# Performance work log

Measured on AMD Instinct MI355X. Metric: run time of the kernel, lower is better.

The kernel has to match this reference:

```python
import jax, jax.numpy as jnp
import numpy as np

WINDOW = 512
OVERLAP = 64
STRIDE = WINDOW - OVERLAP  # 448
HEADS = 12
HEAD_DIM = 3072 // HEADS  # 256
SCALE = 1.0 / np.sqrt(HEAD_DIM)


def setup_inputs() -> dict:
    key = jax.random.key(0)
    ks = jax.random.split(key, 9)
    B, S, H = 1, 8192, 3072
    w = 0.02  # weight init scale
    return {
        "hidden_states": jax.random.normal(ks[0], (B, S, H), jnp.float32),
        "Wq": jax.random.normal(ks[1], (H, H), jnp.float32) * w,
        "bq": jnp.zeros((H,), jnp.float32),
        "Wk": jax.random.normal(ks[2], (H, H), jnp.float32) * w,
        "bk": jnp.zeros((H,), jnp.float32),
        "Wv": jax.random.normal(ks[3], (H, H), jnp.float32) * w,
        "bv": jnp.zeros((H,), jnp.float32),
        "Wo": jax.random.normal(ks[4], (H, H), jnp.float32) * w,
        "bo": jnp.zeros((H,), jnp.float32),
    }


def reference(hidden_states, Wq, bq, Wk, bk, Wv, bv, Wo, bo):
    B, S, H = hidden_states.shape
    n_win = -(-S // STRIDE)  # ceil: windows start at 0, STRIDE, 2*STRIDE, ... < S
    starts = np.arange(n_win) * STRIDE                      # static
    idx = starts[:, None] + np.arange(WINDOW)[None, :]      # [n_win, W]
    valid = jnp.asarray(idx < S)                            # [n_win, W] bool
    idx_c = np.minimum(idx, S - 1)                          # clamp for gather

    # Gather overlapping windows: [B, n_win, W, H] (redundant QKV on overlap, as in original)
    win = hidden_states[:, idx_c]

    def proj(Wm, bm):
        y = jnp.einsum('bnwh,oh->bnwo', win, Wm) + bm
        return y.reshape(B, n_win, WINDOW, HEADS, HEAD_DIM)

    q = proj(Wq, bq)
    k = proj(Wk, bk)
    v = proj(Wv, bv)

    scores = jnp.einsum('bnqhd,bnkhd->bnhqk', q, k) * SCALE  # [B,n_win,heads,W,W]
    # Padded (out-of-range) key positions of the short last window must not attend
    scores = jnp.where(valid[None, :, None, None, :], scores, -1e9)
    attn = jax.nn.softmax(scores, axis=-1)
    ctx = jnp.einsum('bnhqk,bnkhd->bnqhd', attn, v)
    ctx = ctx.reshape(B, n_win, WINDOW, H)
    out_w = jnp.einsum('bnwh,oh->bnwo', ctx, Wo) + bo        # [B,n_win,W,H]

    # zero padded query rows, then overlap-add + average
    out_w = out_w * valid[None, :, :, None].astype(out_w.dtype)
    flat_idx = jnp.asarray(idx_c.reshape(-1))                # [n_win*W]
    output = jnp.zeros((B, S, H), out_w.dtype).at[:, flat_idx].add(
        out_w.reshape(B, -1, H))
    counts = jnp.zeros((S,), out_w.dtype).at[flat_idx].add(
        valid.reshape(-1).astype(out_w.dtype))
    return output / jnp.maximum(counts, 1.0)[None, :, None]
```

## Files before the change

### kernel.cpp

```cpp
#include <hip/hip_runtime.h>
#include <hip/hip_bf16.h>
#include <stdint.h>

#define SEQ   8192
#define HDIM  3072
#define NWIN  19
#define WINL  512
#define STR   448
#define NHEAD 12
#define DHEAD 256
#define QKVN  9216
#define ATTN_SCALE 0.0625f

typedef unsigned short u16;
typedef __bf16 bf16x8 __attribute__((ext_vector_type(8)));
typedef float  f32x4  __attribute__((ext_vector_type(4)));
typedef unsigned short us8 __attribute__((ext_vector_type(8)));

__device__ __forceinline__ u16 f2b(float x) {
  return __builtin_bit_cast(u16, __float2bfloat16(x));
}
__device__ __forceinline__ float b2f(u16 u) {
  return __builtin_bit_cast(float, (unsigned int)(u) << 16);
}
__device__ __forceinline__ void gload_lds16(const void* g, void* l) {
  __builtin_amdgcn_global_load_lds(
      (const __attribute__((address_space(1))) void*)g,
      (__attribute__((address_space(3))) void*)l, 16, 0, 0);
}

__global__ __launch_bounds__(256) void cvt_f32_bf16(const float* __restrict__ src,
                                                    u16* __restrict__ dst, int n8) {
  int i = blockIdx.x * 256 + threadIdx.x;
  if (i >= n8) return;
  const float4* s4 = (const float4*)src;
  float4 a = s4[2 * i], b = s4[2 * i + 1];
  us8 o;
  o[0] = f2b(a.x); o[1] = f2b(a.y); o[2] = f2b(a.z); o[3] = f2b(a.w);
  o[4] = f2b(b.x); o[5] = f2b(b.y); o[6] = f2b(b.z); o[7] = f2b(b.w);
  *((us8*)dst + i) = o;
}

__global__ __launch_bounds__(256) void biascat(const float* __restrict__ bq,
                                               const float* __restrict__ bk,
                                               const float* __restrict__ bv,
                                               float* __restrict__ dst) {
  int i = blockIdx.x * 256 + threadIdx.x;
  if (i >= QKVN) return;
  dst[i] = (i < HDIM) ? bq[i] : ((i < 2 * HDIM) ? bk[i - HDIM] : bv[i - 2 * HDIM]);
}

template <bool BF16OUT>
__global__ __launch_bounds__(512, 2) void gemm256(const u16* __restrict__ A,
                                                  const u16* __restrict__ B,
                                                  const float* __restrict__ bias,
                                                  float* __restrict__ outF,
                                                  u16* __restrict__ outB,
                                                  int N, int K) {
  __shared__ __align__(16) u16 As[4][8192];
  __shared__ __align__(16) u16 Bs[4][8192];
  const int tid = threadIdx.x;
  const int w = tid >> 6, l = tid & 63;
  const int wm = w >> 2, wn = w & 3;
  const int fr = l & 15, g = l >> 4;
  const int xcd = blockIdx.x & 7, loc = blockIdx.x >> 3;
  const int bn = loc >> 2, bm = xcd * 4 + (loc & 3);

  const u16* Ab = A + (size_t)bm * 256 * K;
  const u16* Bb = B + (size_t)bn * 256 * K;

  const int r_st = w * 16 + (l >> 2);
  const int s_st = ((l & 3) ^ ((l >> 3) & 3)) * 8;
  const int sw = (g ^ ((fr >> 1) & 3)) * 8;

  f32x4 acc[8][4];
#pragma unroll
  for (int i = 0; i < 8; ++i)
#pragma unroll
    for (int j = 0; j < 4; ++j) acc[i][j] = (f32x4){0.f, 0.f, 0.f, 0.f};

  auto stA = [&](int T) {
    const int s = T & 3;
#pragma unroll
    for (int h = 0; h < 2; ++h)
      gload_lds16(Ab + (size_t)(h * 128 + r_st) * K + T * 32 + s_st,
                  (char*)&As[s][0] + h * 8192 + w * 1024 + l * 16);
  };
  auto stB = [&](int T) {
    const int s = T & 3;
#pragma unroll
    for (int h = 0; h < 2; ++h)
      gload_lds16(Bb + (size_t)(h * 128 + r_st) * K + T * 32 + s_st,
                  (char*)&Bs[s][0] + h * 8192 + w * 1024 + l * 16);
  };

  stA(0); stB(0); stA(1); stB(1); stA(2); stB(2);
  asm volatile("s_waitcnt vmcnt(8)" ::: "memory");
  __builtin_amdgcn_s_barrier();
  __builtin_amdgcn_sched_barrier(0);

  const int NT = K >> 5;

  auto step = [&](int T, bool doStage, int vm) {
    const u16* as_ = &As[T & 3][0] + (wm * 128 + fr) * 32 + sw;
    const u16* bs_ = &Bs[T & 3][0] + (wn * 64 + fr) * 32 + sw;
    bf16x8 af[8], bf[4];
#pragma unroll
    for (int mi = 0; mi < 4; ++mi) af[mi] = *(const bf16x8*)(as_ + mi * 512);
#pragma unroll
    for (int ni = 0; ni < 4; ++ni) bf[ni] = *(const bf16x8*)(bs_ + ni * 512);
    if (doStage) stA(T + 3);
    __builtin_amdgcn_s_barrier();
    asm volatile("s_waitcnt lgkmcnt(0)" ::: "memory");
    __builtin_amdgcn_s_setprio(1);
#pragma unroll
    for (int mi = 0; mi < 4; ++mi)
#pragma unroll
      for (int ni = 0; ni < 4; ++ni)
        acc[mi][ni] = __builtin_amdgcn_mfma_f32_16x16x32_bf16(af[mi], bf[ni], acc[mi][ni], 0, 0, 0);
    __builtin_amdgcn_s_setprio(0);
    __builtin_amdgcn_s_barrier();
#pragma unroll
    for (int mi = 4; mi < 8; ++mi) af[mi] = *(const bf16x8*)(as_ + mi * 512);
    if (doStage) stB(T + 3);
    __builtin_amdgcn_s_barrier();
    asm volatile("s_waitcnt lgkmcnt(0)" ::: "memory");
    __builtin_amdgcn_s_setprio(1);
#pragma unroll
    for (int mi = 4; mi < 8; ++mi)
#pragma unroll
      for (int ni = 0; ni < 4; ++ni)
        acc[mi][ni] = __builtin_amdgcn_mfma_f32_16x16x32_bf16(af[mi], bf[ni], acc[mi][ni], 0, 0, 0);
    __builtin_amdgcn_s_setprio(0);
    if (vm == 8) asm volatile("s_waitcnt vmcnt(8)" ::: "memory");
    else if (vm == 4) asm volatile("s_waitcnt vmcnt(4)" ::: "memory");
    else if (vm == 0) asm volatile("s_waitcnt vmcnt(0)" ::: "memory");
    __builtin_amdgcn_s_barrier();
    __builtin_amdgcn_sched_barrier(0);
  };

  for (int T = 0; T < NT - 3; ++T) step(T, true, 8);
  step(NT - 3, false, 4);
  step(NT - 2, false, 0);
  step(NT - 1, false, -1);

#pragma unroll
  for (int ni = 0; ni < 4; ++ni) {
    const int c = bn * 256 + wn * 64 + ni * 16 + fr;
    const float bvv = bias ? bias[c] : 0.0f;
#pragma unroll
    for (int mi = 0; mi < 8; ++mi) {
      const int r0 = bm * 256 + wm * 128 + mi * 16 + g * 4;
#pragma unroll
      for (int jj = 0; jj < 4; ++jj) {
        float v = acc[mi][ni][jj] + bvv;
        if (BF16OUT) outB[(size_t)(r0 + jj) * N + c] = f2b(v);
        else         outF[(size_t)(r0 + jj) * N + c] = v;
      }
    }
  }
}

__global__ __launch_bounds__(256) void vtrans(const u16* __restrict__ QKV,
                                              u16* __restrict__ Vt) {
  __shared__ u16 t[64][72];
  const int tid = threadIdx.x;
  const int s0 = blockIdx.x * 64, c0 = blockIdx.y * 64;
  {
    const int r2 = tid >> 3, cc = (tid & 7) * 8;
#pragma unroll
    for (int p = 0; p < 2; ++p) {
      const int row = r2 + p * 32;
      u16 tmp[8];
      *(uint4*)tmp = *(const uint4*)(QKV + (size_t)(s0 + row) * QKVN + 2 * HDIM + c0 + cc);
#pragma unroll
      for (int j = 0; j < 8; ++j) t[row][cc + j] = tmp[j];
    }
  }
  __syncthreads();
  {
    const int cr2 = tid >> 3, sc = tid & 7;
#pragma unroll
    for (int p = 0; p < 2; ++p) {
      const int c = cr2 + p * 32;
      u16 tmp[8];
#pragma unroll
      for (int j = 0; j < 8; ++j) tmp[j] = t[sc * 8 + j][c];
      *(uint4*)(Vt + (size_t)(c0 + c) * SEQ + s0 + sc * 8) = *(uint4*)tmp;
    }
  }
}

__global__ __launch_bounds__(256, 2) void attn_kernel(const u16* __restrict__ QKV,
                                                      const u16* __restrict__ Vt,
                                                      u16* __restrict__ ctxw) {
  __shared__ __align__(16) u16 Ks[64 * 256];
  __shared__ __align__(16) u16 Vts[256 * 64];
  __shared__ __align__(16) u16 Ps[4][16 * 64];
  const int qb = blockIdx.x, h = blockIdx.y, n = blockIdx.z;
  const int tid = threadIdx.x, w = tid >> 6, l = tid & 63;
  const int g = l >> 4, fr = l & 15;
  const int s0 = n * STR;

  bf16x8 qf[8];
  {
    int sq = s0 + qb * 64 + w * 16 + fr;
    if (sq > SEQ - 1) sq = SEQ - 1;
    const u16* qbase = QKV + (size_t)sq * QKVN + h * DHEAD + g * 8;
#pragma unroll
    for (int dc = 0; dc < 8; ++dc) qf[dc] = *(const bf16x8*)(qbase + dc * 32);
  }
  f32x4 ctx[16];
#pragma unroll
  for (int dn = 0; dn < 16; ++dn) ctx[dn] = (f32x4){0.f, 0.f, 0.f, 0.f};
  float mrow[4] = {-3e38f, -3e38f, -3e38f, -3e38f};
  float lrow[4] = {0.f, 0.f, 0.f, 0.f};

  const int kr_in = l >> 5;
  const int kcp = l & 31;
  const int vr_in = l >> 3;
  const int vcp = l & 7;

  for (int kt = 0; kt < 8; ++kt) {
    const int sb = s0 + kt * 64;
#pragma unroll
    for (int i = 0; i < 8; ++i) {
      const int c = i * 4 + w;
      {
        const int krow = c * 2 + kr_in;
        const int cl = kcp ^ (krow & 31);
        int sk = sb + krow;
        if (sk > SEQ - 1) sk = SEQ - 1;
        gload_lds16(QKV + (size_t)sk * QKVN + HDIM + h * DHEAD + cl * 8, (char*)Ks + c * 1024);
      }
      {
        const int d = c * 8 + vr_in;
        const int cl = vcp ^ (d & 7);
        int sv = sb + cl * 8;
        if (sv > SEQ - 8) sv = SEQ - 8;
        gload_lds16(Vt + (size_t)(h * DHEAD + d) * SEQ + sv, (char*)Vts + c * 1024);
      }
    }
    __syncthreads();

    f32x4 sacc[4];
#pragma unroll
    for (int kn = 0; kn < 4; ++kn) sacc[kn] = (f32x4){0.f, 0.f, 0.f, 0.f};
#pragma unroll
    for (int kn = 0; kn < 4; ++kn) {
      const int krow = kn * 16 + fr;
      const char* krp = (const char*)Ks + krow * 512;
      const int rx = krow & 31;
#pragma unroll
      for (int dc = 0; dc < 8; ++dc) {
        bf16x8 kf = *(const bf16x8*)(krp + (((dc * 4 + g) ^ rx) << 4));
        sacc[kn] = __builtin_amdgcn_mfma_f32_16x16x32_bf16(qf[dc], kf, sacc[kn], 0, 0, 0);
      }
    }
    float mt[4];
#pragma unroll
    for (int kn = 0; kn < 4; ++kn) {
      const bool valid = (sb + kn * 16 + fr) < SEQ;
#pragma unroll
      for (int r = 0; r < 4; ++r) {
        float v = valid ? sacc[kn][r] * ATTN_SCALE : -1e9f;
        sacc[kn][r] = v;
        mt[r] = (kn == 0) ? v : fmaxf(mt[r], v);
      }
    }
#pragma unroll
    for (int r = 0; r < 4; ++r) {
#pragma unroll
      for (int off = 1; off < 16; off <<= 1)
        mt[r] = fmaxf(mt[r], __shfl_xor(mt[r], off, 64));
    }
    float corr[4];
#pragma unroll
    for (int r = 0; r < 4; ++r) {
      float mnew = fmaxf(mrow[r], mt[r]);
      corr[r] = __expf(mrow[r] - mnew);
      mrow[r] = mnew;
    }
    float psum[4] = {0.f, 0.f, 0.f, 0.f};
    char* pw = (char*)&Ps[w][0];
#pragma unroll
    for (int kn = 0; kn < 4; ++kn) {
#pragma unroll
      for (int r = 0; r < 4; ++r) {
        float p = __expf(sacc[kn][r] - mrow[r]);
        psum[r] += p;
        const int q = g * 4 + r;
        *(u16*)(pw + q * 128 + ((2 * (kn * 16 + fr)) ^ ((q & 7) << 4))) = f2b(p);
      }
    }
#pragma unroll
    for (int r = 0; r < 4; ++r) {
#pragma unroll
      for (int off = 1; off < 16; off <<= 1)
        psum[r] += __shfl_xor(psum[r], off, 64);
      lrow[r] = lrow[r] * corr[r] + psum[r];
    }
#pragma unroll
    for (int dn = 0; dn < 16; ++dn)
#pragma unroll
      for (int r = 0; r < 4; ++r) ctx[dn][r] *= corr[r];
    __syncthreads();

    bf16x8 pf[2];
#pragma unroll
    for (int kc = 0; kc < 2; ++kc)
      pf[kc] = *(const bf16x8*)(pw + fr * 128 + ((kc * 64 + g * 16) ^ ((fr & 7) << 4)));
#pragma unroll
    for (int dn = 0; dn < 16; ++dn) {
      const int d = dn * 16 + fr;
      const char* vrp = (const char*)Vts + d * 128;
      const int dx = d & 7;
#pragma unroll
      for (int kc = 0; kc < 2; ++kc) {
        bf16x8 vf = *(const bf16x8*)(vrp + (((kc * 4 + g) ^ dx) << 4));
        ctx[dn] = __builtin_amdgcn_mfma_f32_16x16x32_bf16(pf[kc], vf, ctx[dn], 0, 0, 0);
      }
    }
    __syncthreads();
  }
  float inv[4];
#pragma unroll
  for (int r = 0; r < 4; ++r) inv[r] = 1.0f / lrow[r];
  const int qrow0 = qb * 64 + w * 16 + g * 4;
#pragma unroll
  for (int dn = 0; dn < 16; ++dn) {
#pragma unroll
    for (int r = 0; r < 4; ++r) {
      ctxw[(size_t)(n * WINL + qrow0 + r) * HDIM + h * DHEAD + dn * 16 + fr] =
          f2b(ctx[dn][r] * inv[r]);
    }
  }
}

__global__ __launch_bounds__(256) void combine_kernel(const u16* __restrict__ ctxw,
                                                      u16* __restrict__ ctx_avg) {
  int idx = blockIdx.x * 256 + threadIdx.x;
  if (idx >= SEQ * (HDIM / 8)) return;
  const int s = idx / (HDIM / 8);
  const int cc = (idx % (HDIM / 8)) * 8;
  const int w1 = s / STR;
  const int off1 = s - w1 * STR;
  us8 a = *(const us8*)(ctxw + (size_t)(w1 * WINL + off1) * HDIM + cc);
  if (w1 >= 1 && off1 < (WINL - STR)) {
    us8 b = *(const us8*)(ctxw + (size_t)((w1 - 1) * WINL + off1 + STR) * HDIM + cc);
#pragma unroll
    for (int j = 0; j < 8; ++j) a[j] = f2b(0.5f * (b2f(a[j]) + b2f(b[j])));
  }
  *(us8*)(ctx_avg + (size_t)s * HDIM + cc) = a;
}

__global__ void ws_marker(float* out, float v) { out[0] = v; }

extern "C" void kernel_launch(void* const* d_in, const int* in_sizes, int n_in,
                              void* d_out, int out_size, void* d_ws, size_t ws_size,
                              hipStream_t stream) {
  const float* X  = (const float*)d_in[0];
  const float* Wq = (const float*)d_in[1];
  const float* bq = (const float*)d_in[2];
  const float* Wk = (const float*)d_in[3];
  const float* bk = (const float*)d_in[4];
  const float* Wv = (const float*)d_in[5];
  const float* bv = (const float*)d_in[6];
  const float* Wo = (const float*)d_in[7];
  const float* bo = (const float*)d_in[8];
  float* out = (float*)d_out;

  const size_t OFF_XB   = 0;
  const size_t OFF_WQKV = 50331648;
  const size_t OFF_WO   = 106954752;
  const size_t OFF_QKV  = 125829120;
  const size_t OFF_VT   = 276824064;
  const size_t OFF_BIAS = 327155712;
  const size_t WS_NEED  = 327192576;
  if (ws_size < WS_NEED) {
    hipMemsetAsync(d_out, 0, (size_t)out_size * 4, stream);
    ws_marker<<<1, 1, 0, stream>>>(out, (float)(ws_size / 1048576));
    return;
  }
  char* ws = (char*)d_ws;
  u16* Xb      = (u16*)(ws + OFF_XB);
  u16* Wqkvb   = (u16*)(ws + OFF_WQKV);
  u16* Wob     = (u16*)(ws + OFF_WO);
  u16* QKV     = (u16*)(ws + OFF_QKV);
  u16* Vt      = (u16*)(ws + OFF_VT);
  float* biasQ = (float*)(ws + OFF_BIAS);
  u16* ctxw    = (u16*)d_out;
  u16* ctx_avg = Xb;

  cvt_f32_bf16<<<12288, 256, 0, stream>>>(X, Xb, SEQ * HDIM / 8);
  cvt_f32_bf16<<<4608, 256, 0, stream>>>(Wq, Wqkvb, HDIM * HDIM / 8);
  cvt_f32_bf16<<<4608, 256, 0, stream>>>(Wk, Wqkvb + (size_t)HDIM * HDIM, HDIM * HDIM / 8);
  cvt_f32_bf16<<<4608, 256, 0, stream>>>(Wv, Wqkvb + (size_t)2 * HDIM * HDIM, HDIM * HDIM / 8);
  cvt_f32_bf16<<<4608, 256, 0, stream>>>(Wo, Wob, HDIM * HDIM / 8);
  biascat<<<36, 256, 0, stream>>>(bq, bk, bv, biasQ);

  gemm256<true><<<dim3((SEQ / 256) * (QKVN / 256)), 512, 0, stream>>>(
      Xb, Wqkvb, biasQ, nullptr, QKV, QKVN, HDIM);

  vtrans<<<dim3(SEQ / 64, HDIM / 64), 256, 0, stream>>>(QKV, Vt);

  attn_kernel<<<dim3(8, NHEAD, NWIN), 256, 0, stream>>>(QKV, Vt, ctxw);

  combine_kernel<<<12288, 256, 0, stream>>>(ctxw, ctx_avg);

  gemm256<false><<<dim3((SEQ / 256) * (HDIM / 256)), 512, 0, stream>>>(
      ctx_avg, Wob, bo, out, nullptr, HDIM, HDIM);
}
```

Before: 951.2 us.

## Restructure GEMM mainloop to double-buffered 64-wide K tiles with quadrant pipelining

Replaces the 4-stage, 32-wide-K LDS pipeline in the 256x256 GEMM with two buffers of 64-wide K tiles. Each half-tile load is issued between four compute phases over the output quadrants. The warp-to-output mapping becomes interleaved (rows mi*32+wm*16, columns ni*64+wn*16), and the LDS swizzle changes to an XOR over 8 chunks. The goal is fewer barriers per unit of K, more MFMAs per LDS read, and better hiding of global loads. The trade-off is a shallower prefetch depth, which risks exposing memory latency.

Result: faster. 858.8 us (-9.7%).

```diff
diff --git a/kernel.cpp b/kernel.cpp
--- a/kernel.cpp
+++ b/kernel.cpp
@@ -57,8 +57,8 @@
                                                   float* __restrict__ outF,
                                                   u16* __restrict__ outB,
                                                   int N, int K) {
-  __shared__ __align__(16) u16 As[4][8192];
-  __shared__ __align__(16) u16 Bs[4][8192];
+  __shared__ __align__(16) u16 As[2][2][128][64];
+  __shared__ __align__(16) u16 Bs[2][2][128][64];
   const int tid = threadIdx.x;
   const int w = tid >> 6, l = tid & 63;
   const int wm = w >> 2, wn = w & 3;
@@ -66,12 +66,24 @@
   const int xcd = blockIdx.x & 7, loc = blockIdx.x >> 3;
   const int bn = loc >> 2, bm = xcd * 4 + (loc & 3);
 
-  const u16* Ab = A + (size_t)bm * 256 * K;
-  const u16* Bb = B + (size_t)bn * 256 * K;
-
-  const int r_st = w * 16 + (l >> 2);
-  const int s_st = ((l & 3) ^ ((l >> 3) & 3)) * 8;
-  const int sw = (g ^ ((fr >> 1) & 3)) * 8;
+  const int srow = tid >> 3;
+  const int lc = (tid & 7) ^ ((tid >> 3) & 7);
+  const u16* sA0 = A + (size_t)(bm * 256 + srow) * K + lc * 8;
+  const u16* sA1 = sA0 + (size_t)64 * K;
+  const u16* sB0 = B + (size_t)(bn * 256 + srow) * K + lc * 8;
+  const u16* sB1 = sB0 + (size_t)64 * K;
+  const size_t hiK = (size_t)128 * K;
+  const int t16 = tid * 16;
+  char* Aw = (char*)As;
+  char* Bw = (char*)Bs;
+
+  int rbA[4], rbB[2], ck[2];
+#pragma unroll
+  for (int i = 0; i < 4; ++i) rbA[i] = (i * 32 + wm * 16 + fr) * 128;
+  rbB[0] = (wn * 16 + fr) * 128;
+  rbB[1] = (64 + wn * 16 + fr) * 128;
+  ck[0] = ((g) ^ (fr & 7)) * 16;
+  ck[1] = ((4 + g) ^ (fr & 7)) * 16;
 
   f32x4 acc[8][4];
 #pragma unroll
@@ -79,78 +91,116 @@
 #pragma unroll
     for (int j = 0; j < 4; ++j) acc[i][j] = (f32x4){0.f, 0.f, 0.f, 0.f};
 
-  auto stA = [&](int T) {
-    const int s = T & 3;
-#pragma unroll
-    for (int h = 0; h < 2; ++h)
-      gload_lds16(Ab + (size_t)(h * 128 + r_st) * K + T * 32 + s_st,
-                  (char*)&As[s][0] + h * 8192 + w * 1024 + l * 16);
-  };
-  auto stB = [&](int T) {
-    const int s = T & 3;
-#pragma unroll
-    for (int h = 0; h < 2; ++h)
-      gload_lds16(Bb + (size_t)(h * 128 + r_st) * K + T * 32 + s_st,
-                  (char*)&Bs[s][0] + h * 8192 + w * 1024 + l * 16);
-  };
-
-  stA(0); stB(0); stA(1); stB(1); stA(2); stB(2);
-  asm volatile("s_waitcnt vmcnt(8)" ::: "memory");
+  gload_lds16(sA0, Aw + t16); gload_lds16(sA1, Aw + 8192 + t16);
+  gload_lds16(sB0, Bw + t16); gload_lds16(sB1, Bw + 8192 + t16);
+  gload_lds16(sB0 + hiK, Bw + 16384 + t16); gload_lds16(sB1 + hiK, Bw + 16384 + 8192 + t16);
+  gload_lds16(sA0 + hiK, Aw + 16384 + t16); gload_lds16(sA1 + hiK, Aw + 16384 + 8192 + t16);
+  sA0 += 64; sA1 += 64; sB0 += 64; sB1 += 64;
+  asm volatile("s_waitcnt vmcnt(4)" ::: "memory");
   __builtin_amdgcn_s_barrier();
   __builtin_amdgcn_sched_barrier(0);
 
-  const int NT = K >> 5;
-
-  auto step = [&](int T, bool doStage, int vm) {
-    const u16* as_ = &As[T & 3][0] + (wm * 128 + fr) * 32 + sw;
-    const u16* bs_ = &Bs[T & 3][0] + (wn * 64 + fr) * 32 + sw;
-    bf16x8 af[8], bf[4];
-#pragma unroll
-    for (int mi = 0; mi < 4; ++mi) af[mi] = *(const bf16x8*)(as_ + mi * 512);
-#pragma unroll
-    for (int ni = 0; ni < 4; ++ni) bf[ni] = *(const bf16x8*)(bs_ + ni * 512);
-    if (doStage) stA(T + 3);
+  const int NT = K >> 6;
+  for (int T = 0; T < NT; ++T) {
+    const int cur = T & 1, pp = (T + 1) & 1;
+    const bool ds = (T + 1 < NT);
+    const bool last = (T == NT - 1);
+    const char* ah = (const char*)As + cur * 32768;
+    const char* bh = (const char*)Bs + cur * 32768;
+    char* apw = Aw + pp * 32768;
+    char* bpw = Bw + pp * 32768;
+    bf16x8 af[4][2], bf[4][2];
+
+#pragma unroll
+    for (int mi = 0; mi < 4; ++mi)
+#pragma unroll
+      for (int kk = 0; kk < 2; ++kk)
+        af[mi][kk] = *(const bf16x8*)(ah + rbA[mi] + ck[kk]);
+#pragma unroll
+    for (int ni = 0; ni < 2; ++ni)
+#pragma unroll
+      for (int kk = 0; kk < 2; ++kk)
+        bf[ni][kk] = *(const bf16x8*)(bh + rbB[ni] + ck[kk]);
+    if (ds) { gload_lds16(sA0, apw + t16); gload_lds16(sA1, apw + 8192 + t16); }
     __builtin_amdgcn_s_barrier();
     asm volatile("s_waitcnt lgkmcnt(0)" ::: "memory");
     __builtin_amdgcn_s_setprio(1);
 #pragma unroll
-    for (int mi = 0; mi < 4; ++mi)
-#pragma unroll
-      for (int ni = 0; ni < 4; ++ni)
-        acc[mi][ni] = __builtin_amdgcn_mfma_f32_16x16x32_bf16(af[mi], bf[ni], acc[mi][ni], 0, 0, 0);
+    for (int kk = 0; kk < 2; ++kk)
+#pragma unroll
+      for (int mi = 0; mi < 4; ++mi)
+#pragma unroll
+        for (int ni = 0; ni < 2; ++ni)
+          acc[mi][ni] = __builtin_amdgcn_mfma_f32_16x16x32_bf16(af[mi][kk], bf[ni][kk], acc[mi][ni], 0, 0, 0);
     __builtin_amdgcn_s_setprio(0);
-    __builtin_amdgcn_s_barrier();
-#pragma unroll
-    for (int mi = 4; mi < 8; ++mi) af[mi] = *(const bf16x8*)(as_ + mi * 512);
-    if (doStage) stB(T + 3);
+    if (last) asm volatile("s_waitcnt vmcnt(2)" ::: "memory");
+    else      asm volatile("s_waitcnt vmcnt(4)" ::: "memory");
+    __builtin_amdgcn_s_barrier();
+
+#pragma unroll
+    for (int ni = 2; ni < 4; ++ni)
+#pragma unroll
+      for (int kk = 0; kk < 2; ++kk)
+        bf[ni][kk] = *(const bf16x8*)(bh + 16384 + rbB[ni - 2] + ck[kk]);
+    if (ds) { gload_lds16(sB0, bpw + t16); gload_lds16(sB1, bpw + 8192 + t16); }
     __builtin_amdgcn_s_barrier();
     asm volatile("s_waitcnt lgkmcnt(0)" ::: "memory");
     __builtin_amdgcn_s_setprio(1);
 #pragma unroll
-    for (int mi = 4; mi < 8; ++mi)
-#pragma unroll
-      for (int ni = 0; ni < 4; ++ni)
-        acc[mi][ni] = __builtin_amdgcn_mfma_f32_16x16x32_bf16(af[mi], bf[ni], acc[mi][ni], 0, 0, 0);
+    for (int kk = 0; kk < 2; ++kk)
+#pragma unroll
+      for (int mi = 0; mi < 4; ++mi)
+#pragma unroll
+        for (int ni = 2; ni < 4; ++ni)
+          acc[mi][ni] = __builtin_amdgcn_mfma_f32_16x16x32_bf16(af[mi][kk], bf[ni][kk], acc[mi][ni], 0, 0, 0);
     __builtin_amdgcn_s_setprio(0);
-    if (vm == 8) asm volatile("s_waitcnt vmcnt(8)" ::: "memory");
-    else if (vm == 4) asm volatile("s_waitcnt vmcnt(4)" ::: "memory");
-    else if (vm == 0) asm volatile("s_waitcnt vmcnt(0)" ::: "memory");
-    __builtin_amdgcn_s_barrier();
+    if (last) asm volatile("s_waitcnt vmcnt(0)" ::: "memory");
+    else      asm volatile("s_waitcnt vmcnt(4)" ::: "memory");
+    __builtin_amdgcn_s_barrier();
+
+#pragma unroll
+    for (int mi = 0; mi < 4; ++mi)
+#pragma unroll
+      for (int kk = 0; kk < 2; ++kk)
+        af[mi][kk] = *(const bf16x8*)(ah + 16384 + rbA[mi] + ck[kk]);
+    if (ds) { gload_lds16(sB0 + hiK, bpw + 16384 + t16); gload_lds16(sB1 + hiK, bpw + 16384 + 8192 + t16); }
+    __builtin_amdgcn_s_barrier();
+    asm volatile("s_waitcnt lgkmcnt(0)" ::: "memory");
+    __builtin_amdgcn_s_setprio(1);
+#pragma unroll
+    for (int kk = 0; kk < 2; ++kk)
+#pragma unroll
+      for (int mi = 0; mi < 4; ++mi)
+#pragma unroll
+        for (int ni = 0; ni < 2; ++ni)
+          acc[mi + 4][ni] = __builtin_amdgcn_mfma_f32_16x16x32_bf16(af[mi][kk], bf[ni][kk], acc[mi + 4][ni], 0, 0, 0);
+    __builtin_amdgcn_s_setprio(0);
+    __builtin_amdgcn_s_barrier();
+
+    if (ds) { gload_lds16(sA0 + hiK, apw + 16384 + t16); gload_lds16(sA1 + hiK, apw + 16384 + 8192 + t16); }
+    __builtin_amdgcn_s_barrier();
+    __builtin_amdgcn_s_setprio(1);
+#pragma unroll
+    for (int kk = 0; kk < 2; ++kk)
+#pragma unroll
+      for (int mi = 0; mi < 4; ++mi)
+#pragma unroll
+        for (int ni = 2; ni < 4; ++ni)
+          acc[mi + 4][ni] = __builtin_amdgcn_mfma_f32_16x16x32_bf16(af[mi][kk], bf[ni][kk], acc[mi + 4][ni], 0, 0, 0);
+    __builtin_amdgcn_s_setprio(0);
+    if (!last) asm volatile("s_waitcnt vmcnt(4)" ::: "memory");
+    __builtin_amdgcn_s_barrier();
+    if (ds) { sA0 += 64; sA1 += 64; sB0 += 64; sB1 += 64; }
     __builtin_amdgcn_sched_barrier(0);
-  };
-
-  for (int T = 0; T < NT - 3; ++T) step(T, true, 8);
-  step(NT - 3, false, 4);
-  step(NT - 2, false, 0);
-  step(NT - 1, false, -1);
+  }
 
 #pragma unroll
   for (int ni = 0; ni < 4; ++ni) {
-    const int c = bn * 256 + wn * 64 + ni * 16 + fr;
+    const int c = bn * 256 + ni * 64 + wn * 16 + fr;
     const float bvv = bias ? bias[c] : 0.0f;
 #pragma unroll
     for (int mi = 0; mi < 8; ++mi) {
-      const int r0 = bm * 256 + wm * 128 + mi * 16 + g * 4;
+      const int r0 = bm * 256 + mi * 32 + wm * 16 + g * 4;
 #pragma unroll
       for (int jj = 0; jj < 4; ++jj) {
         float v = acc[mi][ni][jj] + bvv;
```

## Restructure GEMM main loop with one barrier per tile and pipelined LDS reads

Applied to the files above, without the earlier changes.

Rewrites the GEMM k-loop so each iteration prefetches global tiles two steps ahead instead of three, cutting the barriers per tile from three to one. LDS fragment reads for the next tile are issued right after that barrier, and the MFMA work is split into four chunks gated by incremental lgkmcnt waits, so LDS reads overlap with matrix math. The aim is to remove barrier stalls and serialized LDS-read latency. The cost is a shallower global prefetch and more registers held across iterations.

Result: faster. 921.5 us (-3.1%).

```diff
diff --git a/kernel.cpp b/kernel.cpp
--- a/kernel.cpp
+++ b/kernel.cpp
@@ -80,69 +80,93 @@
     for (int j = 0; j < 4; ++j) acc[i][j] = (f32x4){0.f, 0.f, 0.f, 0.f};
 
   auto stA = [&](int T) {
-    const int s = T & 3;
-#pragma unroll
-    for (int h = 0; h < 2; ++h)
-      gload_lds16(Ab + (size_t)(h * 128 + r_st) * K + T * 32 + s_st,
-                  (char*)&As[s][0] + h * 8192 + w * 1024 + l * 16);
+    char* d = (char*)&As[T & 3][0] + w * 1024 + l * 16;
+    const u16* s = Ab + (size_t)r_st * K + T * 32 + s_st;
+    gload_lds16(s, d);
+    gload_lds16(s + (size_t)128 * K, d + 8192);
   };
   auto stB = [&](int T) {
-    const int s = T & 3;
-#pragma unroll
-    for (int h = 0; h < 2; ++h)
-      gload_lds16(Bb + (size_t)(h * 128 + r_st) * K + T * 32 + s_st,
-                  (char*)&Bs[s][0] + h * 8192 + w * 1024 + l * 16);
+    char* d = (char*)&Bs[T & 3][0] + w * 1024 + l * 16;
+    const u16* s = Bb + (size_t)r_st * K + T * 32 + s_st;
+    gload_lds16(s, d);
+    gload_lds16(s + (size_t)128 * K, d + 8192);
   };
 
-  stA(0); stB(0); stA(1); stB(1); stA(2); stB(2);
-  asm volatile("s_waitcnt vmcnt(8)" ::: "memory");
+  bf16x8 af[8], bf[4];
+  auto issue_reads = [&](int U) {
+    const u16* as_ = &As[U & 3][0] + (wm * 128 + fr) * 32 + sw;
+    const u16* bs_ = &Bs[U & 3][0] + (wn * 64 + fr) * 32 + sw;
+    af[0] = *(const bf16x8*)(as_);
+    af[1] = *(const bf16x8*)(as_ + 512);
+    bf[0] = *(const bf16x8*)(bs_);
+    bf[1] = *(const bf16x8*)(bs_ + 512);
+    bf[2] = *(const bf16x8*)(bs_ + 1024);
+    bf[3] = *(const bf16x8*)(bs_ + 1536);
+    __builtin_amdgcn_sched_barrier(0);
+    af[2] = *(const bf16x8*)(as_ + 1024);
+    af[3] = *(const bf16x8*)(as_ + 1536);
+    __builtin_amdgcn_sched_barrier(0);
+    af[4] = *(const bf16x8*)(as_ + 2048);
+    af[5] = *(const bf16x8*)(as_ + 2560);
+    __builtin_amdgcn_sched_barrier(0);
+    af[6] = *(const bf16x8*)(as_ + 3072);
+    af[7] = *(const bf16x8*)(as_ + 3584);
+    __builtin_amdgcn_sched_barrier(0);
+  };
+
+  stA(0); stB(0); stA(1); stB(1);
+  asm volatile("s_waitcnt vmcnt(4)" ::: "memory");
   __builtin_amdgcn_s_barrier();
   __builtin_amdgcn_sched_barrier(0);
+  issue_reads(0);
 
   const int NT = K >> 5;
-
-  auto step = [&](int T, bool doStage, int vm) {
-    const u16* as_ = &As[T & 3][0] + (wm * 128 + fr) * 32 + sw;
-    const u16* bs_ = &Bs[T & 3][0] + (wn * 64 + fr) * 32 + sw;
-    bf16x8 af[8], bf[4];
-#pragma unroll
-    for (int mi = 0; mi < 4; ++mi) af[mi] = *(const bf16x8*)(as_ + mi * 512);
-#pragma unroll
-    for (int ni = 0; ni < 4; ++ni) bf[ni] = *(const bf16x8*)(bs_ + ni * 512);
-    if (doStage) stA(T + 3);
-    __builtin_amdgcn_s_barrier();
-    asm volatile("s_waitcnt lgkmcnt(0)" ::: "memory");
+  for (int T = 0; T < NT; ++T) {
+    if (T + 2 < NT) { stA(T + 2); stB(T + 2); }
+    asm volatile("s_waitcnt lgkmcnt(6)" ::: "memory");
+    __builtin_amdgcn_sched_barrier(0);
     __builtin_amdgcn_s_setprio(1);
 #pragma unroll
-    for (int mi = 0; mi < 4; ++mi)
+    for (int mi = 0; mi < 2; ++mi)
 #pragma unroll
       for (int ni = 0; ni < 4; ++ni)
         acc[mi][ni] = __builtin_amdgcn_mfma_f32_16x16x32_bf16(af[mi], bf[ni], acc[mi][ni], 0, 0, 0);
     __builtin_amdgcn_s_setprio(0);
-    __builtin_amdgcn_s_barrier();
-#pragma unroll
-    for (int mi = 4; mi < 8; ++mi) af[mi] = *(const bf16x8*)(as_ + mi * 512);
-    if (doStage) stB(T + 3);
-    __builtin_amdgcn_s_barrier();
-    asm volatile("s_waitcnt lgkmcnt(0)" ::: "memory");
+    asm volatile("s_waitcnt lgkmcnt(4)" ::: "memory");
+    __builtin_amdgcn_sched_barrier(0);
     __builtin_amdgcn_s_setprio(1);
 #pragma unroll
-    for (int mi = 4; mi < 8; ++mi)
+    for (int mi = 2; mi < 4; ++mi)
 #pragma unroll
       for (int ni = 0; ni < 4; ++ni)
         acc[mi][ni] = __builtin_amdgcn_mfma_f32_16x16x32_bf16(af[mi], bf[ni], acc[mi][ni], 0, 0, 0);
     __builtin_amdgcn_s_setprio(0);
-    if (vm == 8) asm volatile("s_waitcnt vmcnt(8)" ::: "memory");
-    else if (vm == 4) asm volatile("s_waitcnt vmcnt(4)" ::: "memory");
-    else if (vm == 0) asm volatile("s_waitcnt vmcnt(0)" ::: "memory");
-    __builtin_amdgcn_s_barrier();
-    __builtin_amdgcn_sched_barrier(0);
-  };
-
-  for (int T = 0; T < NT - 3; ++T) step(T, true, 8);
-  step(NT - 3, false, 4);
-  step(NT - 2, false, 0);
-  step(NT - 1, false, -1);
+    asm volatile("s_waitcnt lgkmcnt(2)" ::: "memory");
+    __builtin_amdgcn_sched_barrier(0);
+    __builtin_amdgcn_s_setprio(1);
+#pragma unroll
+    for (int mi = 4; mi < 6; ++mi)
+#pragma unroll
+      for (int ni = 0; ni < 4; ++ni)
+        acc[mi][ni] = __builtin_amdgcn_mfma_f32_16x16x32_bf16(af[mi], bf[ni], acc[mi][ni], 0, 0, 0);
+    __builtin_amdgcn_s_setprio(0);
+    asm volatile("s_waitcnt lgkmcnt(0)" ::: "memory");
+    __builtin_amdgcn_sched_barrier(0);
+    __builtin_amdgcn_s_setprio(1);
+#pragma unroll
+    for (int mi = 6; mi < 8; ++mi)
+#pragma unroll
+      for (int ni = 0; ni < 4; ++ni)
+        acc[mi][ni] = __builtin_amdgcn_mfma_f32_16x16x32_bf16(af[mi], bf[ni], acc[mi][ni], 0, 0, 0);
+    __builtin_amdgcn_s_setprio(0);
+    if (T < NT - 1) {
+      if (T + 2 < NT) asm volatile("s_waitcnt vmcnt(4)" ::: "memory");
+      else            asm volatile("s_waitcnt vmcnt(0)" ::: "memory");
+      __builtin_amdgcn_s_barrier();
+      __builtin_amdgcn_sched_barrier(0);
+      issue_reads(T + 1);
+    }
+  }
 
 #pragma unroll
   for (int ni = 0; ni < 4; ++ni) {
```
